# Kernel tuning notes

Hardware: AMD Instinct MI355X
Metric: run time of the kernel (lower is better)

Reference implementation:

```python
import jax, jax.numpy as jnp
import numpy as np

B, H, S, D = 4, 16, 2048, 64


def setup_inputs() -> dict:
    key = jax.random.key(0)
    kq, kk, kv = jax.random.split(key, 3)
    q = jax.random.normal(kq, (B, H, S, D), dtype=jnp.float32)
    k = jax.random.normal(kk, (B, H, S, D), dtype=jnp.float32)
    v = jax.random.normal(kv, (B, H, S, D), dtype=jnp.float32)
    # causal mask: 1 where position is masked (j > i), matching mask * -1e9 additive convention
    mask = jnp.triu(jnp.ones((S, S), dtype=jnp.float32), k=1)[None, None]  # [1,1,S,S]
    return {"q": q, "k": k, "v": v, "mask": mask}


def reference(q, k, v, mask):
    scale = 1.0 / jnp.sqrt(jnp.asarray(q.shape[-1], dtype=q.dtype))
    # [B,H,S,S] scores
    scores = jnp.einsum('bhqd,bhkd->bhqk', q, k) * scale
    scores = scores + mask * (-1e9)
    attn = jax.nn.softmax(scores, axis=-1)
    return jnp.einsum('bhqk,bhkd->bhqd', attn, v)
```

## Files before the change

kernel.cpp:

```cpp
#include <hip/hip_runtime.h>
#include <hip/hip_bf16.h>

namespace {

constexpr int Bc = 4, Hc = 16, Sc = 2048, Dc = 64;

using bf16x2 = __attribute__((ext_vector_type(2))) __bf16;
using bf16x8 = __attribute__((ext_vector_type(8))) __bf16;
using f32x4  = __attribute__((ext_vector_type(4))) float;
using f32x16 = __attribute__((ext_vector_type(16))) float;
using uint4v = __attribute__((ext_vector_type(4))) unsigned int;

__device__ __forceinline__ float exp2_hw(float x) {
#if __has_builtin(__builtin_amdgcn_exp2f)
  return __builtin_amdgcn_exp2f(x);
#else
  return exp2f(x);
#endif
}

__device__ __forceinline__ unsigned pk_bf16(float a, float b) {
  bf16x2 t = { (__bf16)a, (__bf16)b };
  return __builtin_bit_cast(unsigned, t);
}

__device__ __forceinline__ void pl32swap(unsigned& a, unsigned& b) {
  asm volatile("s_nop 1\n\tv_permlane32_swap_b32 %0, %1\n\ts_nop 1"
               : "+v"(a), "+v"(b));
}
__device__ __forceinline__ void xhalf_pair(float x, float& lo, float& hi) {
  unsigned a, b;
  asm volatile("v_mov_b32 %0, %2\n\t"
               "v_mov_b32 %1, %2\n\t"
               "s_nop 1\n\t"
               "v_permlane32_swap_b32 %0, %1\n\t"
               "s_nop 1"
               : "=&v"(a), "=&v"(b)
               : "v"(x));
  lo = __builtin_bit_cast(float, a);
  hi = __builtin_bit_cast(float, b);
}
__device__ __forceinline__ float xhalf_sum(float x) {
  float lo, hi; xhalf_pair(x, lo, hi); return lo + hi;
}

__device__ __forceinline__ int vswz(int d) { return ((d >> 4) ^ d) & 7; }

__global__ __launch_bounds__(256, 2)
void fattn_kernel(const float* __restrict__ Q, const float* __restrict__ K,
                  const float* __restrict__ V, float* __restrict__ O) {
  const int tid  = threadIdx.x;
  const int wid  = tid >> 6;
  const int lane = tid & 63;
  const int l31  = lane & 31;
  const int hi   = lane >> 5;

  const int flat = blockIdx.x + 8 * blockIdx.y;
  const int w    = (flat & 7) * 64 + (flat >> 3);
  const int p    = w & 7;
  const int bh   = w >> 3;

  const size_t base = (size_t)bh * (Sc * Dc);
  const float* Qb = Q + base;
  const float* Kb = K + base;
  const float* Vb = V + base;
  float*       Ob = O + base;

  __shared__ __align__(16) __bf16 k_lds[2][64][64];
  __shared__ __align__(16) __bf16 vt_lds[2][64][64];

  const int srow = tid >> 2;
  const int scol = (tid & 3) * 16;
  const int ssw  = (srow & 7) << 3;

  constexpr float QSC = 0.125f * 1.44269504088896f;

  for (int half = 0; half < 2; ++half) {
    const int qp = half ? (15 - p) : p;
    const int qb = qp * 128;
    const int wq = qb + wid * 32;
    const int nkb = 2 * qp + 2;

    bf16x8 qf[4];
    {
      const float* qrow = Qb + (size_t)(wq + l31) * Dc;
      #pragma unroll
      for (int s = 0; s < 4; ++s) {
        const float* src = qrow + s * 16 + hi * 8;
        f32x4 a0 = *(const f32x4*)src;
        f32x4 a1 = *(const f32x4*)(src + 4);
        uint4v wv;
        wv[0] = pk_bf16(a0[0] * QSC, a0[1] * QSC);
        wv[1] = pk_bf16(a0[2] * QSC, a0[3] * QSC);
        wv[2] = pk_bf16(a1[0] * QSC, a1[1] * QSC);
        wv[3] = pk_bf16(a1[2] * QSC, a1[3] * QSC);
        qf[s] = __builtin_bit_cast(bf16x8, wv);
      }
    }

    f32x16 o0, o1;
    #pragma unroll
    for (int i = 0; i < 16; ++i) { o0[i] = 0.f; o1[i] = 0.f; }
    float l = 0.f;

    {
      const float* ksrc = Kb + (size_t)srow * Dc + scol;
      f32x4 a0 = *(const f32x4*)ksrc;
      f32x4 a1 = *(const f32x4*)(ksrc + 4);
      f32x4 a2 = *(const f32x4*)(ksrc + 8);
      f32x4 a3 = *(const f32x4*)(ksrc + 12);
      const float* vsrc = Vb + (size_t)srow * Dc + scol;
      f32x4 b0 = *(const f32x4*)vsrc;
      f32x4 b1 = *(const f32x4*)(vsrc + 4);
      f32x4 b2 = *(const f32x4*)(vsrc + 8);
      f32x4 b3 = *(const f32x4*)(vsrc + 12);
      uint4v w0, w1;
      w0[0] = pk_bf16(a0[0], a0[1]); w0[1] = pk_bf16(a0[2], a0[3]);
      w0[2] = pk_bf16(a1[0], a1[1]); w0[3] = pk_bf16(a1[2], a1[3]);
      w1[0] = pk_bf16(a2[0], a2[1]); w1[1] = pk_bf16(a2[2], a2[3]);
      w1[2] = pk_bf16(a3[0], a3[1]); w1[3] = pk_bf16(a3[2], a3[3]);
      *(uint4v*)&k_lds[0][srow][scol ^ ssw]       = w0;
      *(uint4v*)&k_lds[0][srow][(scol + 8) ^ ssw] = w1;
      f32x4 bb[4] = { b0, b1, b2, b3 };
      #pragma unroll
      for (int c = 0; c < 4; ++c)
        #pragma unroll
        for (int e = 0; e < 4; ++e) {
          const int dd = scol + 4 * c + e;
          vt_lds[0][dd][srow ^ (vswz(dd) << 3)] = (__bf16)bb[c][e];
        }
    }
    __syncthreads();

    for (int t = 0; t < nkb; ++t) {
      const int cur   = t & 1;
      const int kbase = t * 64;
      const bool pre  = (t + 1 < nkb);

      f32x4 a0, a1, a2, a3, b0, b1, b2, b3;
      if (pre) {
        const float* ksrc = Kb + (size_t)(kbase + 64 + srow) * Dc + scol;
        a0 = *(const f32x4*)ksrc;
        a1 = *(const f32x4*)(ksrc + 4);
        a2 = *(const f32x4*)(ksrc + 8);
        a3 = *(const f32x4*)(ksrc + 12);
        const float* vsrc = Vb + (size_t)(kbase + 64 + srow) * Dc + scol;
        b0 = *(const f32x4*)vsrc;
        b1 = *(const f32x4*)(vsrc + 4);
        b2 = *(const f32x4*)(vsrc + 8);
        b3 = *(const f32x4*)(vsrc + 12);
      }

      if (kbase <= wq + 31) {
        const __bf16 (*kc)[64] = k_lds[cur];
        const __bf16 (*vc)[64] = vt_lds[cur];

        f32x16 s0, s1;
        #pragma unroll
        for (int i = 0; i < 16; ++i) { s0[i] = 0.f; s1[i] = 0.f; }
        const int ksw = (l31 & 7) << 3;
        __builtin_amdgcn_s_setprio(1);
        #pragma unroll
        for (int s = 0; s < 4; ++s) {
          bf16x8 kf = *(const bf16x8*)&kc[l31][(s * 16 + hi * 8) ^ ksw];
          s0 = __builtin_amdgcn_mfma_f32_32x32x16_bf16(kf, qf[s], s0, 0, 0, 0);
        }
        #pragma unroll
        for (int s = 0; s < 4; ++s) {
          bf16x8 kf = *(const bf16x8*)&kc[32 + l31][(s * 16 + hi * 8) ^ ksw];
          s1 = __builtin_amdgcn_mfma_f32_32x32x16_bf16(kf, qf[s], s1, 0, 0, 0);
        }
        __builtin_amdgcn_s_setprio(0);

        if (kbase + 63 > wq) {
          const int q   = wq + l31;
          const int dq0 = q - (kbase + 4 * hi);
          const int dq1 = q - (kbase + 32 + 4 * hi);
          #pragma unroll
          for (int i = 0; i < 16; ++i) {
            const int off = (i & 3) + 8 * (i >> 2);
            if (off > dq0) s0[i] = -1e30f;
            if (off > dq1) s1[i] = -1e30f;
          }
        }

        #pragma unroll
        for (int i = 0; i < 16; ++i) {
          s0[i] = exp2_hw(s0[i]);
          s1[i] = exp2_hw(s1[i]);
        }

        float sm[16];
        #pragma unroll
        for (int i = 0; i < 16; ++i) sm[i] = s0[i] + s1[i];
        #pragma unroll
        for (int st = 8; st > 0; st >>= 1)
          #pragma unroll
          for (int i = 0; i < st; ++i) sm[i] += sm[i + st];
        l += xhalf_sum(sm[0]);

        uint4v wv;
        unsigned t0, t1, t2, t3;
        t0 = pk_bf16(s0[0], s0[1]);  t1 = pk_bf16(s0[2], s0[3]);
        t2 = pk_bf16(s0[4], s0[5]);  t3 = pk_bf16(s0[6], s0[7]);
        pl32swap(t0, t2); pl32swap(t1, t3);
        wv[0] = t0; wv[1] = t1; wv[2] = t2; wv[3] = t3;
        const bf16x8 pf0 = __builtin_bit_cast(bf16x8, wv);
        t0 = pk_bf16(s0[8], s0[9]);   t1 = pk_bf16(s0[10], s0[11]);
        t2 = pk_bf16(s0[12], s0[13]); t3 = pk_bf16(s0[14], s0[15]);
        pl32swap(t0, t2); pl32swap(t1, t3);
        wv[0] = t0; wv[1] = t1; wv[2] = t2; wv[3] = t3;
        const bf16x8 pf1 = __builtin_bit_cast(bf16x8, wv);
        t0 = pk_bf16(s1[0], s1[1]);  t1 = pk_bf16(s1[2], s1[3]);
        t2 = pk_bf16(s1[4], s1[5]);  t3 = pk_bf16(s1[6], s1[7]);
        pl32swap(t0, t2); pl32swap(t1, t3);
        wv[0] = t0; wv[1] = t1; wv[2] = t2; wv[3] = t3;
        const bf16x8 pf2 = __builtin_bit_cast(bf16x8, wv);
        t0 = pk_bf16(s1[8], s1[9]);   t1 = pk_bf16(s1[10], s1[11]);
        t2 = pk_bf16(s1[12], s1[13]); t3 = pk_bf16(s1[14], s1[15]);
        pl32swap(t0, t2); pl32swap(t1, t3);
        wv[0] = t0; wv[1] = t1; wv[2] = t2; wv[3] = t3;
        const bf16x8 pf3 = __builtin_bit_cast(bf16x8, wv);

        const int vd0 = l31, vd1 = 32 + l31;
        const int vs0 = vswz(vd0) << 3, vs1 = vswz(vd1) << 3;
        bf16x8 vf;
        __builtin_amdgcn_s_setprio(1);
        vf = *(const bf16x8*)&vc[vd0][(hi * 8) ^ vs0];
        o0 = __builtin_amdgcn_mfma_f32_32x32x16_bf16(vf, pf0, o0, 0, 0, 0);
        vf = *(const bf16x8*)&vc[vd0][(16 + hi * 8) ^ vs0];
        o0 = __builtin_amdgcn_mfma_f32_32x32x16_bf16(vf, pf1, o0, 0, 0, 0);
        vf = *(const bf16x8*)&vc[vd0][(32 + hi * 8) ^ vs0];
        o0 = __builtin_amdgcn_mfma_f32_32x32x16_bf16(vf, pf2, o0, 0, 0, 0);
        vf = *(const bf16x8*)&vc[vd0][(48 + hi * 8) ^ vs0];
        o0 = __builtin_amdgcn_mfma_f32_32x32x16_bf16(vf, pf3, o0, 0, 0, 0);
        vf = *(const bf16x8*)&vc[vd1][(hi * 8) ^ vs1];
        o1 = __builtin_amdgcn_mfma_f32_32x32x16_bf16(vf, pf0, o1, 0, 0, 0);
        vf = *(const bf16x8*)&vc[vd1][(16 + hi * 8) ^ vs1];
        o1 = __builtin_amdgcn_mfma_f32_32x32x16_bf16(vf, pf1, o1, 0, 0, 0);
        vf = *(const bf16x8*)&vc[vd1][(32 + hi * 8) ^ vs1];
        o1 = __builtin_amdgcn_mfma_f32_32x32x16_bf16(vf, pf2, o1, 0, 0, 0);
        vf = *(const bf16x8*)&vc[vd1][(48 + hi * 8) ^ vs1];
        o1 = __builtin_amdgcn_mfma_f32_32x32x16_bf16(vf, pf3, o1, 0, 0, 0);
        __builtin_amdgcn_s_setprio(0);
      }

      if (pre) {
        const int nxt = cur ^ 1;
        uint4v w0, w1;
        w0[0] = pk_bf16(a0[0], a0[1]); w0[1] = pk_bf16(a0[2], a0[3]);
        w0[2] = pk_bf16(a1[0], a1[1]); w0[3] = pk_bf16(a1[2], a1[3]);
        w1[0] = pk_bf16(a2[0], a2[1]); w1[1] = pk_bf16(a2[2], a2[3]);
        w1[2] = pk_bf16(a3[0], a3[1]); w1[3] = pk_bf16(a3[2], a3[3]);
        *(uint4v*)&k_lds[nxt][srow][scol ^ ssw]       = w0;
        *(uint4v*)&k_lds[nxt][srow][(scol + 8) ^ ssw] = w1;
        f32x4 bb[4] = { b0, b1, b2, b3 };
        #pragma unroll
        for (int c = 0; c < 4; ++c)
          #pragma unroll
          for (int e = 0; e < 4; ++e) {
            const int dd = scol + 4 * c + e;
            vt_lds[nxt][dd][srow ^ (vswz(dd) << 3)] = (__bf16)bb[c][e];
          }
      }
      __syncthreads();
    }

    const float inv = 1.0f / l;
    float* orow = Ob + (size_t)(wq + l31) * Dc;
    #pragma unroll
    for (int b = 0; b < 4; ++b) {
      f32x4 u0, u1;
      #pragma unroll
      for (int e = 0; e < 4; ++e) { u0[e] = o0[4 * b + e] * inv; u1[e] = o1[4 * b + e] * inv; }
      *(f32x4*)(orow + 8 * b + 4 * hi)      = u0;
      *(f32x4*)(orow + 32 + 8 * b + 4 * hi) = u1;
    }
    __syncthreads();
  }
}

}

extern "C" void kernel_launch(void* const* d_in, const int* in_sizes, int n_in,
                              void* d_out, int out_size, void* d_ws, size_t ws_size,
                              hipStream_t stream) {
  const float* q = (const float*)d_in[0];
  const float* k = (const float*)d_in[1];
  const float* v = (const float*)d_in[2];
  float* o = (float*)d_out;
  dim3 grid(8, Bc * Hc);
  fattn_kernel<<<grid, dim3(256), 0, stream>>>(q, k, v, o);
}
```

Measured before the change: 65.99 us.

## Software-pipeline QK and PV across iterations with triple-buffered LDS

Restructures the key-block loop so the PV matmul for block t-1 is issued alongside the QK matmul for block t. The softmax and pack work for the current block can then overlap with the previous block's MFMAs. K and V LDS buffers go from double to triple so the V tile from the previous iteration stays live while the next tile is written. The cost is one extra loop iteration, a larger LDS footprint (possible occupancy loss), and P fragments carried in registers across iterations.

```diff
diff --git a/kernel.cpp b/kernel.cpp
--- a/kernel.cpp
+++ b/kernel.cpp
@@ -66,8 +66,8 @@
   const float* Vb = V + base;
   float*       Ob = O + base;
 
-  __shared__ __align__(16) __bf16 k_lds[2][64][64];
-  __shared__ __align__(16) __bf16 vt_lds[2][64][64];
+  __shared__ __align__(16) __bf16 k_lds[3][64][64];
+  __shared__ __align__(16) __bf16 vt_lds[3][64][64];
 
   const int srow = tid >> 2;
   const int scol = (tid & 3) * 16;
@@ -80,6 +80,7 @@
     const int qb = qp * 128;
     const int wq = qb + wid * 32;
     const int nkb = 2 * qp + 2;
+    const int tl  = 2 * qp + (wid >> 1);
 
     bf16x8 qf[4];
     {
@@ -102,6 +103,7 @@
     #pragma unroll
     for (int i = 0; i < 16; ++i) { o0[i] = 0.f; o1[i] = 0.f; }
     float l = 0.f;
+    bf16x8 pfp0, pfp1, pfp2, pfp3;
 
     {
       const float* ksrc = Kb + (size_t)srow * Dc + scol;
@@ -132,9 +134,13 @@
     }
     __syncthreads();
 
-    for (int t = 0; t < nkb; ++t) {
-      const int cur   = t & 1;
+    int bq = 0;
+    for (int t = 0; t <= nkb; ++t) {
+      const int bp = (bq + 2 >= 3) ? bq - 1 : bq + 2;
+      const int bw = (bq + 1 >= 3) ? bq - 2 : bq + 1;
       const int kbase = t * 64;
+      const bool doQK = (t < nkb) && (t <= tl);
+      const bool doPV = (t >= 1) && (t - 1 <= tl);
       const bool pre  = (t + 1 < nkb);
 
       f32x4 a0, a1, a2, a3, b0, b1, b2, b3;
@@ -151,27 +157,51 @@
         b3 = *(const f32x4*)(vsrc + 12);
       }
 
-      if (kbase <= wq + 31) {
-        const __bf16 (*kc)[64] = k_lds[cur];
-        const __bf16 (*vc)[64] = vt_lds[cur];
-
-        f32x16 s0, s1;
+      f32x16 s0, s1;
+      if (doQK) {
         #pragma unroll
         for (int i = 0; i < 16; ++i) { s0[i] = 0.f; s1[i] = 0.f; }
         const int ksw = (l31 & 7) << 3;
         __builtin_amdgcn_s_setprio(1);
         #pragma unroll
         for (int s = 0; s < 4; ++s) {
-          bf16x8 kf = *(const bf16x8*)&kc[l31][(s * 16 + hi * 8) ^ ksw];
+          bf16x8 kf = *(const bf16x8*)&k_lds[bq][l31][(s * 16 + hi * 8) ^ ksw];
           s0 = __builtin_amdgcn_mfma_f32_32x32x16_bf16(kf, qf[s], s0, 0, 0, 0);
         }
         #pragma unroll
         for (int s = 0; s < 4; ++s) {
-          bf16x8 kf = *(const bf16x8*)&kc[32 + l31][(s * 16 + hi * 8) ^ ksw];
+          bf16x8 kf = *(const bf16x8*)&k_lds[bq][32 + l31][(s * 16 + hi * 8) ^ ksw];
           s1 = __builtin_amdgcn_mfma_f32_32x32x16_bf16(kf, qf[s], s1, 0, 0, 0);
         }
         __builtin_amdgcn_s_setprio(0);
-
+      }
+
+      if (doPV) {
+        const int vd0 = l31, vd1 = 32 + l31;
+        const int vs0 = vswz(vd0) << 3, vs1 = vswz(vd1) << 3;
+        const __bf16 (*vc)[64] = vt_lds[bp];
+        bf16x8 vf;
+        __builtin_amdgcn_s_setprio(1);
+        vf = *(const bf16x8*)&vc[vd0][(hi * 8) ^ vs0];
+        o0 = __builtin_amdgcn_mfma_f32_32x32x16_bf16(vf, pfp0, o0, 0, 0, 0);
+        vf = *(const bf16x8*)&vc[vd0][(16 + hi * 8) ^ vs0];
+        o0 = __builtin_amdgcn_mfma_f32_32x32x16_bf16(vf, pfp1, o0, 0, 0, 0);
+        vf = *(const bf16x8*)&vc[vd0][(32 + hi * 8) ^ vs0];
+        o0 = __builtin_amdgcn_mfma_f32_32x32x16_bf16(vf, pfp2, o0, 0, 0, 0);
+        vf = *(const bf16x8*)&vc[vd0][(48 + hi * 8) ^ vs0];
+        o0 = __builtin_amdgcn_mfma_f32_32x32x16_bf16(vf, pfp3, o0, 0, 0, 0);
+        vf = *(const bf16x8*)&vc[vd1][(hi * 8) ^ vs1];
+        o1 = __builtin_amdgcn_mfma_f32_32x32x16_bf16(vf, pfp0, o1, 0, 0, 0);
+        vf = *(const bf16x8*)&vc[vd1][(16 + hi * 8) ^ vs1];
+        o1 = __builtin_amdgcn_mfma_f32_32x32x16_bf16(vf, pfp1, o1, 0, 0, 0);
+        vf = *(const bf16x8*)&vc[vd1][(32 + hi * 8) ^ vs1];
+        o1 = __builtin_amdgcn_mfma_f32_32x32x16_bf16(vf, pfp2, o1, 0, 0, 0);
+        vf = *(const bf16x8*)&vc[vd1][(48 + hi * 8) ^ vs1];
+        o1 = __builtin_amdgcn_mfma_f32_32x32x16_bf16(vf, pfp3, o1, 0, 0, 0);
+        __builtin_amdgcn_s_setprio(0);
+      }
+
+      if (doQK) {
         if (kbase + 63 > wq) {
           const int q   = wq + l31;
           const int dq0 = q - (kbase + 4 * hi);
@@ -183,13 +213,11 @@
             if (off > dq1) s1[i] = -1e30f;
           }
         }
-
         #pragma unroll
         for (int i = 0; i < 16; ++i) {
           s0[i] = exp2_hw(s0[i]);
           s1[i] = exp2_hw(s1[i]);
         }
-
         float sm[16];
         #pragma unroll
         for (int i = 0; i < 16; ++i) sm[i] = s0[i] + s1[i];
@@ -205,65 +233,43 @@
         t2 = pk_bf16(s0[4], s0[5]);  t3 = pk_bf16(s0[6], s0[7]);
         pl32swap(t0, t2); pl32swap(t1, t3);
         wv[0] = t0; wv[1] = t1; wv[2] = t2; wv[3] = t3;
-        const bf16x8 pf0 = __builtin_bit_cast(bf16x8, wv);
+        pfp0 = __builtin_bit_cast(bf16x8, wv);
         t0 = pk_bf16(s0[8], s0[9]);   t1 = pk_bf16(s0[10], s0[11]);
         t2 = pk_bf16(s0[12], s0[13]); t3 = pk_bf16(s0[14], s0[15]);
         pl32swap(t0, t2); pl32swap(t1, t3);
         wv[0] = t0; wv[1] = t1; wv[2] = t2; wv[3] = t3;
-        const bf16x8 pf1 = __builtin_bit_cast(bf16x8, wv);
+        pfp1 = __builtin_bit_cast(bf16x8, wv);
         t0 = pk_bf16(s1[0], s1[1]);  t1 = pk_bf16(s1[2], s1[3]);
         t2 = pk_bf16(s1[4], s1[5]);  t3 = pk_bf16(s1[6], s1[7]);
         pl32swap(t0, t2); pl32swap(t1, t3);
         wv[0] = t0; wv[1] = t1; wv[2] = t2; wv[3] = t3;
-        const bf16x8 pf2 = __builtin_bit_cast(bf16x8, wv);
+        pfp2 = __builtin_bit_cast(bf16x8, wv);
         t0 = pk_bf16(s1[8], s1[9]);   t1 = pk_bf16(s1[10], s1[11]);
         t2 = pk_bf16(s1[12], s1[13]); t3 = pk_bf16(s1[14], s1[15]);
         pl32swap(t0, t2); pl32swap(t1, t3);
         wv[0] = t0; wv[1] = t1; wv[2] = t2; wv[3] = t3;
-        const bf16x8 pf3 = __builtin_bit_cast(bf16x8, wv);
-
-        const int vd0 = l31, vd1 = 32 + l31;
-        const int vs0 = vswz(vd0) << 3, vs1 = vswz(vd1) << 3;
-        bf16x8 vf;
-        __builtin_amdgcn_s_setprio(1);
-        vf = *(const bf16x8*)&vc[vd0][(hi * 8) ^ vs0];
-        o0 = __builtin_amdgcn_mfma_f32_32x32x16_bf16(vf, pf0, o0, 0, 0, 0);
-        vf = *(const bf16x8*)&vc[vd0][(16 + hi * 8) ^ vs0];
-        o0 = __builtin_amdgcn_mfma_f32_32x32x16_bf16(vf, pf1, o0, 0, 0, 0);
-        vf = *(const bf16x8*)&vc[vd0][(32 + hi * 8) ^ vs0];
-        o0 = __builtin_amdgcn_mfma_f32_32x32x16_bf16(vf, pf2, o0, 0, 0, 0);
-        vf = *(const bf16x8*)&vc[vd0][(48 + hi * 8) ^ vs0];
-        o0 = __builtin_amdgcn_mfma_f32_32x32x16_bf16(vf, pf3, o0, 0, 0, 0);
-        vf = *(const bf16x8*)&vc[vd1][(hi * 8) ^ vs1];
-        o1 = __builtin_amdgcn_mfma_f32_32x32x16_bf16(vf, pf0, o1, 0, 0, 0);
-        vf = *(const bf16x8*)&vc[vd1][(16 + hi * 8) ^ vs1];
-        o1 = __builtin_amdgcn_mfma_f32_32x32x16_bf16(vf, pf1, o1, 0, 0, 0);
-        vf = *(const bf16x8*)&vc[vd1][(32 + hi * 8) ^ vs1];
-        o1 = __builtin_amdgcn_mfma_f32_32x32x16_bf16(vf, pf2, o1, 0, 0, 0);
-        vf = *(const bf16x8*)&vc[vd1][(48 + hi * 8) ^ vs1];
-        o1 = __builtin_amdgcn_mfma_f32_32x32x16_bf16(vf, pf3, o1, 0, 0, 0);
-        __builtin_amdgcn_s_setprio(0);
+        pfp3 = __builtin_bit_cast(bf16x8, wv);
       }
 
       if (pre) {
-        const int nxt = cur ^ 1;
         uint4v w0, w1;
         w0[0] = pk_bf16(a0[0], a0[1]); w0[1] = pk_bf16(a0[2], a0[3]);
         w0[2] = pk_bf16(a1[0], a1[1]); w0[3] = pk_bf16(a1[2], a1[3]);
         w1[0] = pk_bf16(a2[0], a2[1]); w1[1] = pk_bf16(a2[2], a2[3]);
         w1[2] = pk_bf16(a3[0], a3[1]); w1[3] = pk_bf16(a3[2], a3[3]);
-        *(uint4v*)&k_lds[nxt][srow][scol ^ ssw]       = w0;
-        *(uint4v*)&k_lds[nxt][srow][(scol + 8) ^ ssw] = w1;
+        *(uint4v*)&k_lds[bw][srow][scol ^ ssw]       = w0;
+        *(uint4v*)&k_lds[bw][srow][(scol + 8) ^ ssw] = w1;
         f32x4 bb[4] = { b0, b1, b2, b3 };
         #pragma unroll
         for (int c = 0; c < 4; ++c)
           #pragma unroll
           for (int e = 0; e < 4; ++e) {
             const int dd = scol + 4 * c + e;
-            vt_lds[nxt][dd][srow ^ (vswz(dd) << 3)] = (__bf16)bb[c][e];
+            vt_lds[bw][dd][srow ^ (vswz(dd) << 3)] = (__bf16)bb[c][e];
           }
       }
-      __syncthreads();
+      if (t < nkb) __syncthreads();
+      bq = bw;
     }
 
     const float inv = 1.0f / l;
```

After: 64.10 us. -2.9%, faster.

## Process KV tiles in pairs to halve block barriers per iteration

Applied to the files above, without the earlier changes.

Double-buffers pairs of 64-row K/V tiles in LDS (doubling shared memory to 64KB) so each loop iteration computes two tiles and only one __syncthreads is needed per pair. Global loads for the next pair are interleaved with compute of the current tiles. The aim is to cut barrier count and improve overlap, at the cost of more LDS use, which may reduce occupancy.

```diff
diff --git a/kernel.cpp b/kernel.cpp
--- a/kernel.cpp
+++ b/kernel.cpp
@@ -66,20 +66,52 @@
   const float* Vb = V + base;
   float*       Ob = O + base;
 
-  __shared__ __align__(16) __bf16 k_lds[2][64][64];
-  __shared__ __align__(16) __bf16 vt_lds[2][64][64];
+  __shared__ __align__(16) __bf16 k_lds[2][2][64][64];
+  __shared__ __align__(16) __bf16 vt_lds[2][2][64][64];
 
   const int srow = tid >> 2;
   const int scol = (tid & 3) * 16;
   const int ssw  = (srow & 7) << 3;
 
   constexpr float QSC = 0.125f * 1.44269504088896f;
+
+  f32x4 Rk0, Rk1, Rk2, Rk3, Rv0, Rv1, Rv2, Rv3;
+
+  auto issue_loads = [&](int krow) {
+    const float* ksrc = Kb + (size_t)(krow + srow) * Dc + scol;
+    Rk0 = *(const f32x4*)ksrc;
+    Rk1 = *(const f32x4*)(ksrc + 4);
+    Rk2 = *(const f32x4*)(ksrc + 8);
+    Rk3 = *(const f32x4*)(ksrc + 12);
+    const float* vsrc = Vb + (size_t)(krow + srow) * Dc + scol;
+    Rv0 = *(const f32x4*)vsrc;
+    Rv1 = *(const f32x4*)(vsrc + 4);
+    Rv2 = *(const f32x4*)(vsrc + 8);
+    Rv3 = *(const f32x4*)(vsrc + 12);
+  };
+  auto write_stage = [&](__bf16 (*kd)[64], __bf16 (*vd)[64]) {
+    uint4v w0, w1;
+    w0[0] = pk_bf16(Rk0[0], Rk0[1]); w0[1] = pk_bf16(Rk0[2], Rk0[3]);
+    w0[2] = pk_bf16(Rk1[0], Rk1[1]); w0[3] = pk_bf16(Rk1[2], Rk1[3]);
+    w1[0] = pk_bf16(Rk2[0], Rk2[1]); w1[1] = pk_bf16(Rk2[2], Rk2[3]);
+    w1[2] = pk_bf16(Rk3[0], Rk3[1]); w1[3] = pk_bf16(Rk3[2], Rk3[3]);
+    *(uint4v*)&kd[srow][scol ^ ssw]       = w0;
+    *(uint4v*)&kd[srow][(scol + 8) ^ ssw] = w1;
+    #pragma unroll
+    for (int e = 0; e < 4; ++e) {
+      vd[scol + e     ][srow ^ (vswz(scol + e     ) << 3)] = (__bf16)Rv0[e];
+      vd[scol + 4 + e ][srow ^ (vswz(scol + 4 + e ) << 3)] = (__bf16)Rv1[e];
+      vd[scol + 8 + e ][srow ^ (vswz(scol + 8 + e ) << 3)] = (__bf16)Rv2[e];
+      vd[scol + 12 + e][srow ^ (vswz(scol + 12 + e) << 3)] = (__bf16)Rv3[e];
+    }
+  };
 
   for (int half = 0; half < 2; ++half) {
     const int qp = half ? (15 - p) : p;
     const int qb = qp * 128;
     const int wq = qb + wid * 32;
     const int nkb = 2 * qp + 2;
+    const int npair = qp + 1;
 
     bf16x8 qf[4];
     {
@@ -103,166 +135,118 @@
     for (int i = 0; i < 16; ++i) { o0[i] = 0.f; o1[i] = 0.f; }
     float l = 0.f;
 
-    {
-      const float* ksrc = Kb + (size_t)srow * Dc + scol;
-      f32x4 a0 = *(const f32x4*)ksrc;
-      f32x4 a1 = *(const f32x4*)(ksrc + 4);
-      f32x4 a2 = *(const f32x4*)(ksrc + 8);
-      f32x4 a3 = *(const f32x4*)(ksrc + 12);
-      const float* vsrc = Vb + (size_t)srow * Dc + scol;
-      f32x4 b0 = *(const f32x4*)vsrc;
-      f32x4 b1 = *(const f32x4*)(vsrc + 4);
-      f32x4 b2 = *(const f32x4*)(vsrc + 8);
-      f32x4 b3 = *(const f32x4*)(vsrc + 12);
-      uint4v w0, w1;
-      w0[0] = pk_bf16(a0[0], a0[1]); w0[1] = pk_bf16(a0[2], a0[3]);
-      w0[2] = pk_bf16(a1[0], a1[1]); w0[3] = pk_bf16(a1[2], a1[3]);
-      w1[0] = pk_bf16(a2[0], a2[1]); w1[1] = pk_bf16(a2[2], a2[3]);
-      w1[2] = pk_bf16(a3[0], a3[1]); w1[3] = pk_bf16(a3[2], a3[3]);
-      *(uint4v*)&k_lds[0][srow][scol ^ ssw]       = w0;
-      *(uint4v*)&k_lds[0][srow][(scol + 8) ^ ssw] = w1;
-      f32x4 bb[4] = { b0, b1, b2, b3 };
-      #pragma unroll
-      for (int c = 0; c < 4; ++c)
-        #pragma unroll
-        for (int e = 0; e < 4; ++e) {
-          const int dd = scol + 4 * c + e;
-          vt_lds[0][dd][srow ^ (vswz(dd) << 3)] = (__bf16)bb[c][e];
-        }
-    }
-    __syncthreads();
-
-    for (int t = 0; t < nkb; ++t) {
-      const int cur   = t & 1;
-      const int kbase = t * 64;
-      const bool pre  = (t + 1 < nkb);
-
-      f32x4 a0, a1, a2, a3, b0, b1, b2, b3;
-      if (pre) {
-        const float* ksrc = Kb + (size_t)(kbase + 64 + srow) * Dc + scol;
-        a0 = *(const f32x4*)ksrc;
-        a1 = *(const f32x4*)(ksrc + 4);
-        a2 = *(const f32x4*)(ksrc + 8);
-        a3 = *(const f32x4*)(ksrc + 12);
-        const float* vsrc = Vb + (size_t)(kbase + 64 + srow) * Dc + scol;
-        b0 = *(const f32x4*)vsrc;
-        b1 = *(const f32x4*)(vsrc + 4);
-        b2 = *(const f32x4*)(vsrc + 8);
-        b3 = *(const f32x4*)(vsrc + 12);
-      }
-
-      if (kbase <= wq + 31) {
-        const __bf16 (*kc)[64] = k_lds[cur];
-        const __bf16 (*vc)[64] = vt_lds[cur];
-
-        f32x16 s0, s1;
-        #pragma unroll
-        for (int i = 0; i < 16; ++i) { s0[i] = 0.f; s1[i] = 0.f; }
-        const int ksw = (l31 & 7) << 3;
-        __builtin_amdgcn_s_setprio(1);
-        #pragma unroll
-        for (int s = 0; s < 4; ++s) {
-          bf16x8 kf = *(const bf16x8*)&kc[l31][(s * 16 + hi * 8) ^ ksw];
-          s0 = __builtin_amdgcn_mfma_f32_32x32x16_bf16(kf, qf[s], s0, 0, 0, 0);
-        }
-        #pragma unroll
-        for (int s = 0; s < 4; ++s) {
-          bf16x8 kf = *(const bf16x8*)&kc[32 + l31][(s * 16 + hi * 8) ^ ksw];
-          s1 = __builtin_amdgcn_mfma_f32_32x32x16_bf16(kf, qf[s], s1, 0, 0, 0);
-        }
-        __builtin_amdgcn_s_setprio(0);
-
-        if (kbase + 63 > wq) {
-          const int q   = wq + l31;
-          const int dq0 = q - (kbase + 4 * hi);
-          const int dq1 = q - (kbase + 32 + 4 * hi);
-          #pragma unroll
-          for (int i = 0; i < 16; ++i) {
-            const int off = (i & 3) + 8 * (i >> 2);
-            if (off > dq0) s0[i] = -1e30f;
-            if (off > dq1) s1[i] = -1e30f;
-          }
-        }
-
+    auto compute_tile = [&](int kbase, const __bf16 (*kc)[64],
+                            const __bf16 (*vc)[64]) {
+      f32x16 s0, s1;
+      #pragma unroll
+      for (int i = 0; i < 16; ++i) { s0[i] = 0.f; s1[i] = 0.f; }
+      const int ksw = (l31 & 7) << 3;
+      __builtin_amdgcn_s_setprio(1);
+      #pragma unroll
+      for (int s = 0; s < 4; ++s) {
+        bf16x8 kf = *(const bf16x8*)&kc[l31][(s * 16 + hi * 8) ^ ksw];
+        s0 = __builtin_amdgcn_mfma_f32_32x32x16_bf16(kf, qf[s], s0, 0, 0, 0);
+      }
+      #pragma unroll
+      for (int s = 0; s < 4; ++s) {
+        bf16x8 kf = *(const bf16x8*)&kc[32 + l31][(s * 16 + hi * 8) ^ ksw];
+        s1 = __builtin_amdgcn_mfma_f32_32x32x16_bf16(kf, qf[s], s1, 0, 0, 0);
+      }
+      __builtin_amdgcn_s_setprio(0);
+
+      if (kbase + 63 > wq) {
+        const int q   = wq + l31;
+        const int dq0 = q - (kbase + 4 * hi);
+        const int dq1 = q - (kbase + 32 + 4 * hi);
         #pragma unroll
         for (int i = 0; i < 16; ++i) {
-          s0[i] = exp2_hw(s0[i]);
-          s1[i] = exp2_hw(s1[i]);
+          const int off = (i & 3) + 8 * (i >> 2);
+          if (off > dq0) s0[i] = -1e30f;
+          if (off > dq1) s1[i] = -1e30f;
         }
-
-        float sm[16];
+      }
+
+      #pragma unroll
+      for (int i = 0; i < 16; ++i) {
+        s0[i] = exp2_hw(s0[i]);
+        s1[i] = exp2_hw(s1[i]);
+      }
+      float sm[16];
+      #pragma unroll
+      for (int i = 0; i < 16; ++i) sm[i] = s0[i] + s1[i];
+      #pragma unroll
+      for (int st = 8; st > 0; st >>= 1)
         #pragma unroll
-        for (int i = 0; i < 16; ++i) sm[i] = s0[i] + s1[i];
-        #pragma unroll
-        for (int st = 8; st > 0; st >>= 1)
-          #pragma unroll
-          for (int i = 0; i < st; ++i) sm[i] += sm[i + st];
-        l += xhalf_sum(sm[0]);
-
-        uint4v wv;
-        unsigned t0, t1, t2, t3;
-        t0 = pk_bf16(s0[0], s0[1]);  t1 = pk_bf16(s0[2], s0[3]);
-        t2 = pk_bf16(s0[4], s0[5]);  t3 = pk_bf16(s0[6], s0[7]);
-        pl32swap(t0, t2); pl32swap(t1, t3);
-        wv[0] = t0; wv[1] = t1; wv[2] = t2; wv[3] = t3;
-        const bf16x8 pf0 = __builtin_bit_cast(bf16x8, wv);
-        t0 = pk_bf16(s0[8], s0[9]);   t1 = pk_bf16(s0[10], s0[11]);
-        t2 = pk_bf16(s0[12], s0[13]); t3 = pk_bf16(s0[14], s0[15]);
-        pl32swap(t0, t2); pl32swap(t1, t3);
-        wv[0] = t0; wv[1] = t1; wv[2] = t2; wv[3] = t3;
-        const bf16x8 pf1 = __builtin_bit_cast(bf16x8, wv);
-        t0 = pk_bf16(s1[0], s1[1]);  t1 = pk_bf16(s1[2], s1[3]);
-        t2 = pk_bf16(s1[4], s1[5]);  t3 = pk_bf16(s1[6], s1[7]);
-        pl32swap(t0, t2); pl32swap(t1, t3);
-        wv[0] = t0; wv[1] = t1; wv[2] = t2; wv[3] = t3;
-        const bf16x8 pf2 = __builtin_bit_cast(bf16x8, wv);
-        t0 = pk_bf16(s1[8], s1[9]);   t1 = pk_bf16(s1[10], s1[11]);
-        t2 = pk_bf16(s1[12], s1[13]); t3 = pk_bf16(s1[14], s1[15]);
-        pl32swap(t0, t2); pl32swap(t1, t3);
-        wv[0] = t0; wv[1] = t1; wv[2] = t2; wv[3] = t3;
-        const bf16x8 pf3 = __builtin_bit_cast(bf16x8, wv);
-
-        const int vd0 = l31, vd1 = 32 + l31;
-        const int vs0 = vswz(vd0) << 3, vs1 = vswz(vd1) << 3;
-        bf16x8 vf;
-        __builtin_amdgcn_s_setprio(1);
-        vf = *(const bf16x8*)&vc[vd0][(hi * 8) ^ vs0];
-        o0 = __builtin_amdgcn_mfma_f32_32x32x16_bf16(vf, pf0, o0, 0, 0, 0);
-        vf = *(const bf16x8*)&vc[vd0][(16 + hi * 8) ^ vs0];
-        o0 = __builtin_amdgcn_mfma_f32_32x32x16_bf16(vf, pf1, o0, 0, 0, 0);
-        vf = *(const bf16x8*)&vc[vd0][(32 + hi * 8) ^ vs0];
-        o0 = __builtin_amdgcn_mfma_f32_32x32x16_bf16(vf, pf2, o0, 0, 0, 0);
-        vf = *(const bf16x8*)&vc[vd0][(48 + hi * 8) ^ vs0];
-        o0 = __builtin_amdgcn_mfma_f32_32x32x16_bf16(vf, pf3, o0, 0, 0, 0);
-        vf = *(const bf16x8*)&vc[vd1][(hi * 8) ^ vs1];
-        o1 = __builtin_amdgcn_mfma_f32_32x32x16_bf16(vf, pf0, o1, 0, 0, 0);
-        vf = *(const bf16x8*)&vc[vd1][(16 + hi * 8) ^ vs1];
-        o1 = __builtin_amdgcn_mfma_f32_32x32x16_bf16(vf, pf1, o1, 0, 0, 0);
-        vf = *(const bf16x8*)&vc[vd1][(32 + hi * 8) ^ vs1];
-        o1 = __builtin_amdgcn_mfma_f32_32x32x16_bf16(vf, pf2, o1, 0, 0, 0);
-        vf = *(const bf16x8*)&vc[vd1][(48 + hi * 8) ^ vs1];
-        o1 = __builtin_amdgcn_mfma_f32_32x32x16_bf16(vf, pf3, o1, 0, 0, 0);
-        __builtin_amdgcn_s_setprio(0);
-      }
-
-      if (pre) {
-        const int nxt = cur ^ 1;
-        uint4v w0, w1;
-        w0[0] = pk_bf16(a0[0], a0[1]); w0[1] = pk_bf16(a0[2], a0[3]);
-        w0[2] = pk_bf16(a1[0], a1[1]); w0[3] = pk_bf16(a1[2], a1[3]);
-        w1[0] = pk_bf16(a2[0], a2[1]); w1[1] = pk_bf16(a2[2], a2[3]);
-        w1[2] = pk_bf16(a3[0], a3[1]); w1[3] = pk_bf16(a3[2], a3[3]);
-        *(uint4v*)&k_lds[nxt][srow][scol ^ ssw]       = w0;
-        *(uint4v*)&k_lds[nxt][srow][(scol + 8) ^ ssw] = w1;
-        f32x4 bb[4] = { b0, b1, b2, b3 };
-        #pragma unroll
-        for (int c = 0; c < 4; ++c)
-          #pragma unroll
-          for (int e = 0; e < 4; ++e) {
-            const int dd = scol + 4 * c + e;
-            vt_lds[nxt][dd][srow ^ (vswz(dd) << 3)] = (__bf16)bb[c][e];
-          }
-      }
+        for (int i = 0; i < st; ++i) sm[i] += sm[i + st];
+      l += xhalf_sum(sm[0]);
+
+      uint4v wv;
+      unsigned t0, t1, t2, t3;
+      t0 = pk_bf16(s0[0], s0[1]);  t1 = pk_bf16(s0[2], s0[3]);
+      t2 = pk_bf16(s0[4], s0[5]);  t3 = pk_bf16(s0[6], s0[7]);
+      pl32swap(t0, t2); pl32swap(t1, t3);
+      wv[0] = t0; wv[1] = t1; wv[2] = t2; wv[3] = t3;
+      const bf16x8 pf0 = __builtin_bit_cast(bf16x8, wv);
+      t0 = pk_bf16(s0[8], s0[9]);   t1 = pk_bf16(s0[10], s0[11]);
+      t2 = pk_bf16(s0[12], s0[13]); t3 = pk_bf16(s0[14], s0[15]);
+      pl32swap(t0, t2); pl32swap(t1, t3);
+      wv[0] = t0; wv[1] = t1; wv[2] = t2; wv[3] = t3;
+      const bf16x8 pf1 = __builtin_bit_cast(bf16x8, wv);
+      t0 = pk_bf16(s1[0], s1[1]);  t1 = pk_bf16(s1[2], s1[3]);
+      t2 = pk_bf16(s1[4], s1[5]);  t3 = pk_bf16(s1[6], s1[7]);
+      pl32swap(t0, t2); pl32swap(t1, t3);
+      wv[0] = t0; wv[1] = t1; wv[2] = t2; wv[3] = t3;
+      const bf16x8 pf2 = __builtin_bit_cast(bf16x8, wv);
+      t0 = pk_bf16(s1[8], s1[9]);   t1 = pk_bf16(s1[10], s1[11]);
+      t2 = pk_bf16(s1[12], s1[13]); t3 = pk_bf16(s1[14], s1[15]);
+      pl32swap(t0, t2); pl32swap(t1, t3);
+      wv[0] = t0; wv[1] = t1; wv[2] = t2; wv[3] = t3;
+      const bf16x8 pf3 = __builtin_bit_cast(bf16x8, wv);
+
+      const int vd0 = l31, vd1 = 32 + l31;
+      const int vs0 = vswz(vd0) << 3, vs1 = vswz(vd1) << 3;
+      bf16x8 vf;
+      __builtin_amdgcn_s_setprio(1);
+      vf = *(const bf16x8*)&vc[vd0][(hi * 8) ^ vs0];
+      o0 = __builtin_amdgcn_mfma_f32_32x32x16_bf16(vf, pf0, o0, 0, 0, 0);
+      vf = *(const bf16x8*)&vc[vd0][(16 + hi * 8) ^ vs0];
+      o0 = __builtin_amdgcn_mfma_f32_32x32x16_bf16(vf, pf1, o0, 0, 0, 0);
+      vf = *(const bf16x8*)&vc[vd0][(32 + hi * 8) ^ vs0];
+      o0 = __builtin_amdgcn_mfma_f32_32x32x16_bf16(vf, pf2, o0, 0, 0, 0);
+      vf = *(const bf16x8*)&vc[vd0][(48 + hi * 8) ^ vs0];
+      o0 = __builtin_amdgcn_mfma_f32_32x32x16_bf16(vf, pf3, o0, 0, 0, 0);
+      vf = *(const bf16x8*)&vc[vd1][(hi * 8) ^ vs1];
+      o1 = __builtin_amdgcn_mfma_f32_32x32x16_bf16(vf, pf0, o1, 0, 0, 0);
+      vf = *(const bf16x8*)&vc[vd1][(16 + hi * 8) ^ vs1];
+      o1 = __builtin_amdgcn_mfma_f32_32x32x16_bf16(vf, pf1, o1, 0, 0, 0);
+      vf = *(const bf16x8*)&vc[vd1][(32 + hi * 8) ^ vs1];
+      o1 = __builtin_amdgcn_mfma_f32_32x32x16_bf16(vf, pf2, o1, 0, 0, 0);
+      vf = *(const bf16x8*)&vc[vd1][(48 + hi * 8) ^ vs1];
+      o1 = __builtin_amdgcn_mfma_f32_32x32x16_bf16(vf, pf3, o1, 0, 0, 0);
+      __builtin_amdgcn_s_setprio(0);
+    };
+
+    issue_loads(0);
+    write_stage(k_lds[0][0], vt_lds[0][0]);
+    issue_loads(64);
+    write_stage(k_lds[0][1], vt_lds[0][1]);
+    __syncthreads();
+
+    for (int u = 0; u < npair; ++u) {
+      const int pp = u & 1, np = pp ^ 1;
+      const int a  = 2 * u;
+      const bool stg = (a + 2 < nkb);
+
+      if (stg) issue_loads((a + 2) * 64);
+      if (a * 64 <= wq + 31)
+        compute_tile(a * 64, k_lds[pp][0], vt_lds[pp][0]);
+      if (stg) {
+        write_stage(k_lds[np][0], vt_lds[np][0]);
+        issue_loads((a + 3) * 64);
+      }
+      if ((a + 1) * 64 <= wq + 31)
+        compute_tile((a + 1) * 64, k_lds[pp][1], vt_lds[pp][1]);
+      if (stg) write_stage(k_lds[np][1], vt_lds[np][1]);
       __syncthreads();
     }
 
```

Measured after the change: 75.87 us. +15.0%, slower.
